# Performance work log

Hardware: AMD Instinct MI355X
Metric: run time of the kernel (lower is better)

Reference implementation:

```python
import jax, jax.numpy as jnp
import numpy as np

RADIUS = 0.5
NSAMPLE = 32
RATIO = 0.25
HEADS = 8


def _ln(x, g, b, eps=1e-5):
    m = x.mean(-1, keepdims=True)
    v = ((x - m) ** 2).mean(-1, keepdims=True)
    return (x - m) / jnp.sqrt(v + eps) * g + b


def _fps(xyz, M):
    """Farthest point sampling (start at index 0, matches pytorch3d default). Non-differentiable."""
    xyz = jax.lax.stop_gradient(xyz)  # mirrors @torch.no_grad
    B, N, _ = xyz.shape

    def step(carry, _):
        mind, last = carry  # (B,N), (B,)
        lastp = jnp.take_along_axis(xyz, last[:, None, None], axis=1)  # (B,1,3)
        d = jnp.sum((xyz - lastp) ** 2, axis=-1)  # (B,N)
        mind = jnp.minimum(mind, d)
        nxt = jnp.argmax(mind, axis=1).astype(jnp.int32)
        return (mind, nxt), last

    init = (jnp.full((B, N), jnp.inf, xyz.dtype), jnp.zeros((B,), jnp.int32))
    _, idx = jax.lax.scan(step, init, None, length=M)
    return idx.T  # (B,M)


def setup_inputs() -> dict:
    key = jax.random.key(0)
    ks = jax.random.split(key, 12)
    B, N, Cin, C = 2, 8192, 64, 128
    w = lambda i, shape: jax.random.normal(ks[i], shape, jnp.float32) * 0.02
    return {
        "xyz": jax.random.normal(ks[0], (B, N, 3), jnp.float32),
        "feats": jax.random.normal(ks[1], (B, N, Cin), jnp.float32),
        "W_in": w(2, (Cin, C)), "b_in": jnp.zeros((C,), jnp.float32),
        "ln_in_g": jnp.ones((C,), jnp.float32), "ln_in_b": jnp.zeros((C,), jnp.float32),
        "W_pos": w(3, (3, C)), "b_pos": jnp.zeros((C,), jnp.float32),
        "Wq": w(4, (C, C)), "bq": jnp.zeros((C,), jnp.float32),
        "Wk": w(5, (C, C)), "bk": jnp.zeros((C,), jnp.float32),
        "Wv": w(6, (C, C)), "bv": jnp.zeros((C,), jnp.float32),
        "Wo": w(7, (C, C)), "bo": jnp.zeros((C,), jnp.float32),
        "ln1_g": jnp.ones((C,), jnp.float32), "ln1_b": jnp.zeros((C,), jnp.float32),
        "W1": w(8, (C, 4 * C)), "b1": jnp.zeros((4 * C,), jnp.float32),
        "W2": w(9, (4 * C, C)), "b2": jnp.zeros((C,), jnp.float32),
        "ln2_g": jnp.ones((C,), jnp.float32), "ln2_b": jnp.zeros((C,), jnp.float32),
        "out_g": jnp.ones((C,), jnp.float32), "out_b": jnp.zeros((C,), jnp.float32),
    }


def reference(xyz, feats, W_in, b_in, ln_in_g, ln_in_b, W_pos, b_pos,
              Wq, bq, Wk, bk, Wv, bv, Wo, bo, ln1_g, ln1_b,
              W1, b1, W2, b2, ln2_g, ln2_b, out_g, out_b):
    B, N, _ = xyz.shape
    M = max(1, int(round(N * RATIO)))
    K = NSAMPLE

    # --- FPS centroids ---
    ctr_idx = _fps(xyz, M)  # (B,M) int32
    ctr_xyz = xyz[jnp.arange(B)[:, None], ctr_idx]  # (B,M,3)

    # --- ball query: first K points (by index) within radius; -1 where missing ---
    d2 = jnp.sum((ctr_xyz[:, :, None, :] - xyz[:, None, :, :]) ** 2, axis=-1)  # (B,M,N)
    within = d2 < RADIUS * RADIUS
    cand = jnp.where(within, jnp.arange(N, dtype=jnp.int32)[None, None, :], N)
    first_k = jnp.sort(cand, axis=-1)[..., :K]  # (B,M,K)
    raw_idx = jnp.where(first_k < N, first_k, -1)
    neigh_idx = jnp.where(raw_idx < 0, ctr_idx[:, :, None], raw_idx)  # fill pads with centroid

    b3 = jnp.arange(B)[:, None, None]
    neigh_xyz = xyz[b3, neigh_idx]     # (B,M,K,3)
    neigh_feats = feats[b3, neigh_idx]  # (B,M,K,Cin)

    # --- in_proj: Linear -> LayerNorm -> ReLU ---
    h = jax.nn.relu(_ln(neigh_feats @ W_in + b_in, ln_in_g, ln_in_b))  # (B,M,K,C)
    C = h.shape[-1]
    BM = B * M
    pad = (raw_idx < 0).reshape(BM, K)  # key padding mask

    # --- local transformer layer (coords -> positional embedding, post-norm) ---
    x = h.reshape(BM, K, C) + (neigh_xyz.reshape(BM, K, 3) @ W_pos + b_pos)
    H = HEADS
    Dh = C // H
    split = lambda t: t.reshape(BM, K, H, Dh).transpose(0, 2, 1, 3)  # (BM,H,K,Dh)
    q, k, v = split(x @ Wq + bq), split(x @ Wk + bk), split(x @ Wv + bv)
    scores = jnp.einsum('bhqd,bhkd->bhqk', q, k) / np.sqrt(Dh)
    scores = jnp.where(pad[:, None, None, :], -1e9, scores)
    attn = jax.nn.softmax(scores, axis=-1)
    o = jnp.einsum('bhqk,bhkd->bhqd', attn, v).transpose(0, 2, 1, 3).reshape(BM, K, C)
    x = _ln(x + o @ Wo + bo, ln1_g, ln1_b)
    x = _ln(x + jax.nn.relu(x @ W1 + b1) @ W2 + b2, ln2_g, ln2_b)

    # --- max-pool over neighbourhood, out LayerNorm ---
    pooled = _ln(x.max(axis=1).reshape(B, M, C), out_g, out_b)
    return ctr_xyz, pooled
```

## Files before the change

kernel.cpp:

```cpp
#include <hip/hip_runtime.h>
#include <math.h>

#define N_PTS 8192
#define BATCH 2
#define M_CTR 2048
#define KNB   32
#define CIN   64
#define CH    128
#define NHEAD 8
#define DH    16

typedef __attribute__((ext_vector_type(4))) float f32x4;
typedef __attribute__((ext_vector_type(8))) short bf16x8;

template<int CTRL>
__device__ __forceinline__ unsigned long long dpp_max_u64(unsigned long long k) {
  int lo = (int)(unsigned)k;
  int hi = (int)(k >> 32);
  int lo2 = __builtin_amdgcn_update_dpp(0, lo, CTRL, 0xF, 0xF, true);
  int hi2 = __builtin_amdgcn_update_dpp(0, hi, CTRL, 0xF, 0xF, true);
  unsigned long long o = ((unsigned long long)(unsigned)hi2 << 32) | (unsigned)lo2;
  return o > k ? o : k;
}

__device__ __forceinline__ unsigned long long swz16_max_u64(unsigned long long k) {
  int lo = (int)(unsigned)k;
  int hi = (int)(k >> 32);
  int lo2 = __builtin_amdgcn_ds_swizzle(lo, 0x401F);
  int hi2 = __builtin_amdgcn_ds_swizzle(hi, 0x401F);
  unsigned long long o = ((unsigned long long)(unsigned)hi2 << 32) | (unsigned)lo2;
  return o > k ? o : k;
}

__device__ __forceinline__ unsigned long long maxu64(unsigned long long a,
                                                     unsigned long long b) {
  return a > b ? a : b;
}

__global__ __launch_bounds__(1024, 1) void fps_kernel(const float* __restrict__ xyz,
                                                      int* __restrict__ ctrIdx,
                                                      float* __restrict__ outCtr) {
  __shared__ float4 sxyz[N_PTS];
  __shared__ unsigned long long redK[4];

  const int b = blockIdx.x;
  const int t = threadIdx.x;
  const int lane = t & 63;
  const float* xb = xyz + (size_t)b * N_PTS * 3;

  float px[8], py[8], pz[8], mind[8];
  unsigned lo8[8];
#pragma unroll
  for (int s = 0; s < 8; ++s) {
    int pt = t + s * 1024;
    float x = xb[pt * 3 + 0];
    float y = xb[pt * 3 + 1];
    float z = xb[pt * 3 + 2];
    px[s] = x; py[s] = y; pz[s] = z;
    mind[s] = INFINITY;
    lo8[s] = ~(unsigned)pt;
    sxyz[pt] = make_float4(x, y, z, 0.f);
  }
  if (t < 3) redK[t] = 0ull;
  __syncthreads();

  int last = 0;
  for (int m = 0; m < M_CTR; ++m) {
    float4 lp = sxyz[last];
    if (t == 0) {
      ctrIdx[b * M_CTR + m] = last;
      float* o = outCtr + (size_t)(b * M_CTR + m) * 3;
      o[0] = lp.x; o[1] = lp.y; o[2] = lp.z;
    }
    unsigned long long c0 = 0ull, c1 = 0ull;
#pragma unroll
    for (int s = 0; s < 8; ++s) {
      float dx = __fsub_rn(px[s], lp.x);
      float dy = __fsub_rn(py[s], lp.y);
      float dz = __fsub_rn(pz[s], lp.z);
      float d2 = __fadd_rn(__fadd_rn(__fmul_rn(dx, dx), __fmul_rn(dy, dy)),
                           __fmul_rn(dz, dz));
      float mn = fminf(mind[s], d2);
      mind[s] = mn;
      unsigned long long key =
          ((unsigned long long)__float_as_uint(mn) << 32) | lo8[s];
      if (s & 1) c1 = maxu64(c1, key); else c0 = maxu64(c0, key);
    }
    unsigned long long k0 = maxu64(c0, c1);
    k0 = dpp_max_u64<0xB1>(k0);
    k0 = dpp_max_u64<0x4E>(k0);
    k0 = dpp_max_u64<0x141>(k0);
    k0 = dpp_max_u64<0x140>(k0);
    k0 = swz16_max_u64(k0);
    const int buf = m % 3;
    if ((lane & 31) == 0)
      atomicMax((unsigned long long*)&redK[buf], k0);
    if (t == 1) redK[(m + 1) % 3] = 0ull;
    __syncthreads();
    last = (int)(~(unsigned)redK[buf]);
  }
}

__global__ __launch_bounds__(256) void ballq_kernel(const float* __restrict__ xyz,
                                                    const int* __restrict__ ctrIdx,
                                                    int* __restrict__ rawIdx) {
  const int cm   = blockIdx.x * 4 + (threadIdx.x >> 6);
  const int lane = threadIdx.x & 63;
  const int b    = cm >> 11;
  const float* xb = xyz + (size_t)b * N_PTS * 3;
  const int ci = ctrIdx[cm];
  const float cx = xb[ci * 3 + 0], cy = xb[ci * 3 + 1], cz = xb[ci * 3 + 2];
  int* out = rawIdx + (size_t)cm * KNB;
  int have = 0;
  for (int base = 0; base < N_PTS; base += 64) {
    int pt = base + lane;
    float dx = __fsub_rn(cx, xb[pt * 3 + 0]);
    float dy = __fsub_rn(cy, xb[pt * 3 + 1]);
    float dz = __fsub_rn(cz, xb[pt * 3 + 2]);
    float d2 = __fadd_rn(__fadd_rn(__fmul_rn(dx, dx), __fmul_rn(dy, dy)),
                         __fmul_rn(dz, dz));
    bool hit = d2 < 0.25f;
    unsigned long long mask = __ballot(hit);
    if (hit) {
      int rank = have + __popcll(mask & ((1ull << lane) - 1ull));
      if (rank < KNB) out[rank] = pt;
    }
    have += __popcll(mask);
    if (have >= KNB) break;
  }
  if (lane < KNB && lane >= have) out[lane] = -1;
}

__device__ __forceinline__ unsigned short f2bf(float f) {
  unsigned u = __float_as_uint(f);
  unsigned r = (u + 0x7FFFu + ((u >> 16) & 1u)) >> 16;
  return (unsigned short)r;
}
__device__ __forceinline__ float bf2f(unsigned short s) {
  return __uint_as_float(((unsigned)s) << 16);
}

__global__ __launch_bounds__(256) void prep_kernel(const float* __restrict__ W_in,
    const float* __restrict__ Wq, const float* __restrict__ Wk,
    const float* __restrict__ Wv, const float* __restrict__ Wo,
    const float* __restrict__ W1, const float* __restrict__ W2,
    short* __restrict__ wsW) {
  int i = blockIdx.x * 256 + threadIdx.x;
  if (i >= 204800) return;
  const float* src; int K, C, off;
  if (i < 8192)        { src = W_in; K = 64;  C = 128; off = i; }
  else if (i < 24576)  { src = Wq;   K = 128; C = 128; off = i - 8192; }
  else if (i < 40960)  { src = Wk;   K = 128; C = 128; off = i - 24576; }
  else if (i < 57344)  { src = Wv;   K = 128; C = 128; off = i - 40960; }
  else if (i < 73728)  { src = Wo;   K = 128; C = 128; off = i - 57344; }
  else if (i < 139264) { src = W1;   K = 128; C = 512; off = i - 73728; }
  else                 { src = W2;   K = 512; C = 128; off = i - 139264; }
  int c = off / K, k = off - c * K;
  wsW[i] = (short)f2bf(src[(size_t)k * C + c]);
}

#define XS  136
#define VTS 40
#define PS  264

struct SAParams {
  const float* xyz; const float* feats;
  const float* b_in; const float* ln_in_g; const float* ln_in_b;
  const float* W_pos; const float* b_pos;
  const float* bq; const float* bk; const float* bv; const float* bo;
  const float* ln1_g; const float* ln1_b;
  const float* b1; const float* b2;
  const float* ln2_g; const float* ln2_b; const float* out_g; const float* out_b;
  const short* wsW;
  const int* ctrIdx; const int* rawIdx;
  float* out;
};

template<int C>
__device__ __forceinline__ float dppf(float v) {
  return __int_as_float(__builtin_amdgcn_update_dpp(0, __float_as_int(v), C, 0xF, 0xF, true));
}
__device__ __forceinline__ float red16_add(float v) {
  v += dppf<0xB1>(v);  v += dppf<0x4E>(v);
  v += dppf<0x141>(v); v += dppf<0x140>(v);
  return v;
}
__device__ __forceinline__ float red16_max(float v) {
  v = fmaxf(v, dppf<0xB1>(v));  v = fmaxf(v, dppf<0x4E>(v));
  v = fmaxf(v, dppf<0x141>(v)); v = fmaxf(v, dppf<0x140>(v));
  return v;
}

template<int NCT, int NKS>
__device__ __forceinline__ void mm_mfma(const short* __restrict__ albase, int lstr,
                                        const short* __restrict__ wt, int wK,
                                        f32x4 (&acc)[NCT], int l15, int lg) {
#pragma unroll
  for (int ks = 0; ks < NKS; ++ks) {
    bf16x8 a = *(const bf16x8*)(albase + l15 * lstr + ks * 32 + lg * 8);
#pragma unroll
    for (int ct = 0; ct < NCT; ++ct) {
      bf16x8 bf = *(const bf16x8*)(wt + (size_t)(ct * 16 + l15) * wK + ks * 32 + lg * 8);
      acc[ct] = __builtin_amdgcn_mfma_f32_16x16x32_bf16(a, bf, acc[ct], 0, 0, 0);
    }
  }
}

__global__ __launch_bounds__(128, 1) void sa_kernel(SAParams p) {
  __shared__ short sm[3 * 32 * XS + 128 * VTS + 32 * PS];
  __shared__ float nxs[32], nys[32], nzs[32];
  __shared__ int   nidx[32];
  __shared__ unsigned padmaskS;
  __shared__ float psum[2][2];

  short* const xb  = sm;
  short* const qb  = sm + 32 * XS;
  short* const kb  = sm + 2 * 32 * XS;
  short* const vT  = sm + 3 * 32 * XS;
  short* const Pb  = sm + 3 * 32 * XS + 128 * VTS;
  short* const fsb = Pb;
  short* const ob  = qb;
  short* const hb  = kb;

  const int t    = threadIdx.x;
  const int lane = t & 63;
  const int rt   = t >> 6;
  const int l15  = lane & 15;
  const int lg   = lane >> 4;
  const int cm   = blockIdx.x;
  const int b    = cm >> 11;
  const short* arow = 0;

  if (t < 32) {
    int raw = p.rawIdx[(size_t)cm * KNB + t];
    int ci  = p.ctrIdx[cm];
    int ni  = (raw < 0) ? ci : raw;
    nidx[t] = ni;
    const float* q = p.xyz + ((size_t)b * N_PTS + ni) * 3;
    nxs[t] = q[0]; nys[t] = q[1]; nzs[t] = q[2];
  }
  if (t < 64) {
    bool isPad = (t < 32) ? (p.rawIdx[(size_t)cm * KNB + t] < 0) : false;
    unsigned long long m = __ballot(isPad);
    if (t == 0) padmaskS = (unsigned)m;
  }
  __syncthreads();

  {
    int row = t >> 2;
    int cs  = (t & 3) * 16;
    const float* src = p.feats + ((size_t)b * N_PTS + nidx[row]) * CIN + cs;
    float4 f0 = *(const float4*)(src + 0);
    float4 f1 = *(const float4*)(src + 4);
    float4 f2 = *(const float4*)(src + 8);
    float4 f3 = *(const float4*)(src + 12);
    unsigned short u[16];
#pragma unroll
    for (int j = 0; j < 4; ++j) {
      u[j]      = f2bf((&f0.x)[j]); u[4 + j]  = f2bf((&f1.x)[j]);
      u[8 + j]  = f2bf((&f2.x)[j]); u[12 + j] = f2bf((&f3.x)[j]);
    }
    unsigned packed[8];
#pragma unroll
    for (int j = 0; j < 8; ++j) packed[j] = (unsigned)u[2 * j] | ((unsigned)u[2 * j + 1] << 16);
    uint4 w0 = make_uint4(packed[0], packed[1], packed[2], packed[3]);
    uint4 w1 = make_uint4(packed[4], packed[5], packed[6], packed[7]);
    *(uint4*)(fsb + row * 72 + cs)     = w0;
    *(uint4*)(fsb + row * 72 + cs + 8) = w1;
  }
  __syncthreads();

  const unsigned padmask = padmaskS;
  float rowxyz[3][4];
#pragma unroll
  for (int r = 0; r < 4; ++r) {
    int row = rt * 16 + lg * 4 + r;
    rowxyz[0][r] = nxs[row]; rowxyz[1][r] = nys[row]; rowxyz[2][r] = nzs[row];
  }

  {
    f32x4 acc[8] = {};
    mm_mfma<8, 2>(fsb + rt * 16 * 72, 72, p.wsW + 0, 64, acc, l15, lg);
    float s[4] = {}, sq[4] = {};
#pragma unroll
    for (int ct = 0; ct < 8; ++ct) {
      float bia = p.b_in[ct * 16 + l15];
#pragma unroll
      for (int r = 0; r < 4; ++r) {
        acc[ct][r] += bia;
        s[r] += acc[ct][r]; sq[r] += acc[ct][r] * acc[ct][r];
      }
    }
    float mean[4], inv[4];
#pragma unroll
    for (int r = 0; r < 4; ++r) {
      float S = red16_add(s[r]), SQ = red16_add(sq[r]);
      mean[r] = S * (1.0f / CH);
      float var = fmaxf(SQ * (1.0f / CH) - mean[r] * mean[r], 0.f);
      inv[r] = rsqrtf(var + 1e-5f);
    }
#pragma unroll
    for (int ct = 0; ct < 8; ++ct) {
      int c = ct * 16 + l15;
      float g  = p.ln_in_g[c], bt = p.ln_in_b[c];
      float w0 = p.W_pos[0 * CH + c], w1 = p.W_pos[1 * CH + c];
      float w2 = p.W_pos[2 * CH + c], bp = p.b_pos[c];
#pragma unroll
      for (int r = 0; r < 4; ++r) {
        int row = rt * 16 + lg * 4 + r;
        float h = (acc[ct][r] - mean[r]) * inv[r] * g + bt;
        h = fmaxf(h, 0.f);
        float pos = fmaf(rowxyz[0][r], w0, fmaf(rowxyz[1][r], w1,
                    fmaf(rowxyz[2][r], w2, bp)));
        xb[row * XS + c] = (short)f2bf(h + pos);
      }
    }
  }
  __syncthreads();

  arow = xb + rt * 16 * XS;
  {
    f32x4 acc[8] = {};
    mm_mfma<8, 4>(arow, XS, p.wsW + 8192, 128, acc, l15, lg);
#pragma unroll
    for (int ct = 0; ct < 8; ++ct) {
      int c = ct * 16 + l15;
      float bia = p.bq[c];
#pragma unroll
      for (int r = 0; r < 4; ++r)
        qb[(rt * 16 + lg * 4 + r) * XS + c] = (short)f2bf((acc[ct][r] + bia) * 0.25f);
    }
  }
  {
    f32x4 acc[8] = {};
    mm_mfma<8, 4>(arow, XS, p.wsW + 24576, 128, acc, l15, lg);
#pragma unroll
    for (int ct = 0; ct < 8; ++ct) {
      int c = ct * 16 + l15;
      float bia = p.bk[c];
#pragma unroll
      for (int r = 0; r < 4; ++r)
        kb[(rt * 16 + lg * 4 + r) * XS + c] = (short)f2bf(acc[ct][r] + bia);
    }
  }
  {
    f32x4 acc[8] = {};
    mm_mfma<8, 4>(arow, XS, p.wsW + 40960, 128, acc, l15, lg);
#pragma unroll
    for (int ct = 0; ct < 8; ++ct) {
      int c = ct * 16 + l15;
      float bia = p.bv[c];
#pragma unroll
      for (int r = 0; r < 4; ++r)
        vT[c * VTS + rt * 16 + lg * 4 + r] = (short)f2bf(acc[ct][r] + bia);
    }
  }
  __syncthreads();

  {
    bool pad0 = (padmask >> l15) & 1u;
    bool pad1 = (padmask >> (16 + l15)) & 1u;
    const bf16x8 z = {0, 0, 0, 0, 0, 0, 0, 0};
#pragma unroll
    for (int h = 0; h < NHEAD; ++h) {
      bf16x8 a = *(const bf16x8*)(qb + (rt * 16 + l15) * XS + h * DH + (lg & 1) * 8);
      if (lg >= 2) a = z;
      bf16x8 b0 = *(const bf16x8*)(kb + (l15) * XS + h * DH + (lg & 1) * 8);
      bf16x8 b1 = *(const bf16x8*)(kb + (16 + l15) * XS + h * DH + (lg & 1) * 8);
      f32x4 s0 = {}, s1 = {};
      s0 = __builtin_amdgcn_mfma_f32_16x16x32_bf16(a, b0, s0, 0, 0, 0);
      s1 = __builtin_amdgcn_mfma_f32_16x16x32_bf16(a, b1, s1, 0, 0, 0);
#pragma unroll
      for (int r = 0; r < 4; ++r) {
        float v0 = pad0 ? -1e9f : s0[r];
        float v1 = pad1 ? -1e9f : s1[r];
        float mx = red16_max(fmaxf(v0, v1));
        float e0 = __expf(v0 - mx), e1 = __expf(v1 - mx);
        float sum = red16_add(e0 + e1);
        float isum = 1.0f / sum;
        int row = rt * 16 + lg * 4 + r;
        Pb[row * PS + h * 32 + l15]      = (short)f2bf(e0 * isum);
        Pb[row * PS + h * 32 + 16 + l15] = (short)f2bf(e1 * isum);
      }
    }
  }
  __syncthreads();

  {
#pragma unroll
    for (int h = 0; h < NHEAD; ++h) {
      bf16x8 a  = *(const bf16x8*)(Pb + (rt * 16 + l15) * PS + h * 32 + lg * 8);
      bf16x8 bf = *(const bf16x8*)(vT + (h * DH + l15) * VTS + lg * 8);
      f32x4 o = {};
      o = __builtin_amdgcn_mfma_f32_16x16x32_bf16(a, bf, o, 0, 0, 0);
#pragma unroll
      for (int r = 0; r < 4; ++r)
        ob[(rt * 16 + lg * 4 + r) * XS + h * DH + l15] = (short)f2bf(o[r]);
    }
  }

  {
    f32x4 acc[8] = {};
    mm_mfma<8, 4>(ob + rt * 16 * XS, XS, p.wsW + 57344, 128, acc, l15, lg);
    float s[4] = {}, sq[4] = {};
#pragma unroll
    for (int ct = 0; ct < 8; ++ct) {
      int c = ct * 16 + l15;
      float bia = p.bo[c];
#pragma unroll
      for (int r = 0; r < 4; ++r) {
        int row = rt * 16 + lg * 4 + r;
        acc[ct][r] += bia + bf2f((unsigned short)xb[row * XS + c]);
        s[r] += acc[ct][r]; sq[r] += acc[ct][r] * acc[ct][r];
      }
    }
    float mean[4], inv[4];
#pragma unroll
    for (int r = 0; r < 4; ++r) {
      float S = red16_add(s[r]), SQ = red16_add(sq[r]);
      mean[r] = S * (1.0f / CH);
      float var = fmaxf(SQ * (1.0f / CH) - mean[r] * mean[r], 0.f);
      inv[r] = rsqrtf(var + 1e-5f);
    }
#pragma unroll
    for (int ct = 0; ct < 8; ++ct) {
      int c = ct * 16 + l15;
      float g = p.ln1_g[c], bt = p.ln1_b[c];
#pragma unroll
      for (int r = 0; r < 4; ++r) {
        int row = rt * 16 + lg * 4 + r;
        xb[row * XS + c] = (short)f2bf((acc[ct][r] - mean[r]) * inv[r] * g + bt);
      }
    }
  }

  {
    f32x4 acc2[8] = {};
#pragma unroll
    for (int cb = 0; cb < 4; ++cb) {
      f32x4 acch[8] = {};
      mm_mfma<8, 4>(xb + rt * 16 * XS, XS, p.wsW + 73728 + cb * 128 * 128, 128,
                    acch, l15, lg);
#pragma unroll
      for (int ct = 0; ct < 8; ++ct) {
        int c = ct * 16 + l15;
        float bia = p.b1[cb * 128 + c];
#pragma unroll
        for (int r = 0; r < 4; ++r)
          hb[(rt * 16 + lg * 4 + r) * XS + c] = (short)f2bf(fmaxf(acch[ct][r] + bia, 0.f));
      }
      __syncthreads();
      mm_mfma<8, 4>(hb + rt * 16 * XS, XS, p.wsW + 139264 + cb * 128, 512,
                    acc2, l15, lg);
      __syncthreads();
    }
    float s[4] = {}, sq[4] = {};
#pragma unroll
    for (int ct = 0; ct < 8; ++ct) {
      int c = ct * 16 + l15;
      float bia = p.b2[c];
#pragma unroll
      for (int r = 0; r < 4; ++r) {
        int row = rt * 16 + lg * 4 + r;
        acc2[ct][r] += bia + bf2f((unsigned short)xb[row * XS + c]);
        s[r] += acc2[ct][r]; sq[r] += acc2[ct][r] * acc2[ct][r];
      }
    }
    float mean[4], inv[4];
#pragma unroll
    for (int r = 0; r < 4; ++r) {
      float S = red16_add(s[r]), SQ = red16_add(sq[r]);
      mean[r] = S * (1.0f / CH);
      float var = fmaxf(SQ * (1.0f / CH) - mean[r] * mean[r], 0.f);
      inv[r] = rsqrtf(var + 1e-5f);
    }
#pragma unroll
    for (int ct = 0; ct < 8; ++ct) {
      int c = ct * 16 + l15;
      float g = p.ln2_g[c], bt = p.ln2_b[c];
#pragma unroll
      for (int r = 0; r < 4; ++r) {
        int row = rt * 16 + lg * 4 + r;
        xb[row * XS + c] = (short)f2bf((acc2[ct][r] - mean[r]) * inv[r] * g + bt);
      }
    }
  }
  __syncthreads();

  {
    float mx = -INFINITY;
#pragma unroll 8
    for (int r = 0; r < KNB; ++r) mx = fmaxf(mx, bf2f((unsigned short)xb[r * XS + t]));
    float s = mx, sq = mx * mx;
#pragma unroll
    for (int off = 1; off < 64; off <<= 1) {
      s  += __shfl_xor(s,  off, 64);
      sq += __shfl_xor(sq, off, 64);
    }
    if (lane == 0) { psum[rt][0] = s; psum[rt][1] = sq; }
    __syncthreads();
    float S = psum[0][0] + psum[1][0];
    float SQ = psum[0][1] + psum[1][1];
    float mean = S * (1.0f / CH);
    float var = fmaxf(SQ * (1.0f / CH) - mean * mean, 0.f);
    float inv = rsqrtf(var + 1e-5f);
    p.out[(size_t)BATCH * M_CTR * 3 + (size_t)cm * CH + t] =
        (mx - mean) * inv * p.out_g[t] + p.out_b[t];
  }
}

extern "C" void kernel_launch(void* const* d_in, const int* in_sizes, int n_in,
                              void* d_out, int out_size, void* d_ws, size_t ws_size,
                              hipStream_t stream) {
  const float* xyz     = (const float*)d_in[0];
  const float* feats   = (const float*)d_in[1];
  const float* W_in    = (const float*)d_in[2];
  const float* b_in    = (const float*)d_in[3];
  const float* ln_in_g = (const float*)d_in[4];
  const float* ln_in_b = (const float*)d_in[5];
  const float* W_pos   = (const float*)d_in[6];
  const float* b_pos   = (const float*)d_in[7];
  const float* Wq      = (const float*)d_in[8];
  const float* bq      = (const float*)d_in[9];
  const float* Wk      = (const float*)d_in[10];
  const float* bk      = (const float*)d_in[11];
  const float* Wv      = (const float*)d_in[12];
  const float* bv      = (const float*)d_in[13];
  const float* Wo      = (const float*)d_in[14];
  const float* bo      = (const float*)d_in[15];
  const float* ln1_g   = (const float*)d_in[16];
  const float* ln1_b   = (const float*)d_in[17];
  const float* W1      = (const float*)d_in[18];
  const float* b1      = (const float*)d_in[19];
  const float* W2      = (const float*)d_in[20];
  const float* b2      = (const float*)d_in[21];
  const float* ln2_g   = (const float*)d_in[22];
  const float* ln2_b   = (const float*)d_in[23];
  const float* out_g   = (const float*)d_in[24];
  const float* out_b   = (const float*)d_in[25];
  float* out = (float*)d_out;

  int* wsCtr = (int*)d_ws;
  int* wsRaw = wsCtr + BATCH * M_CTR;
  short* wsW = (short*)(wsRaw + BATCH * M_CTR * KNB);

  prep_kernel<<<(204800 + 255) / 256, 256, 0, stream>>>(W_in, Wq, Wk, Wv, Wo,
                                                        W1, W2, wsW);
  fps_kernel<<<BATCH, 1024, 0, stream>>>(xyz, wsCtr, out);
  ballq_kernel<<<(BATCH * M_CTR) / 4, 256, 0, stream>>>(xyz, wsCtr, wsRaw);

  SAParams p{xyz, feats, b_in, ln_in_g, ln_in_b, W_pos, b_pos,
             bq, bk, bv, bo, ln1_g, ln1_b, b1, b2,
             ln2_g, ln2_b, out_g, out_b,
             wsW, wsCtr, wsRaw, out};
  sa_kernel<<<BATCH * M_CTR, 128, 0, stream>>>(p);
}
```

Measured before the change: 2.638 ms.

## Rework FPS argmax reduction with 32-bit wave reductions and per-wave LDS slots

Replaces the 64-bit packed-key DPP reduction and shared-memory atomicMax in farthest point sampling with two 32-bit wave reductions: a float max, then a min over indices among lanes holding that max. Each wave writes one packed candidate to a double-buffered LDS array, and every thread reduces the 8 candidates itself after the barrier. The block shrinks to 512 threads with 16 points per thread. The intent is to shorten the serial per-iteration critical path of the 2048 dependent FPS steps (fewer atomics, cheaper shuffles, fewer waves at the barrier), at the cost of more per-thread distance work and register use.

```diff
diff --git a/kernel.cpp b/kernel.cpp
--- a/kernel.cpp
+++ b/kernel.cpp
@@ -14,54 +14,49 @@
 typedef __attribute__((ext_vector_type(8))) short bf16x8;
 
 template<int CTRL>
-__device__ __forceinline__ unsigned long long dpp_max_u64(unsigned long long k) {
-  int lo = (int)(unsigned)k;
-  int hi = (int)(k >> 32);
-  int lo2 = __builtin_amdgcn_update_dpp(0, lo, CTRL, 0xF, 0xF, true);
-  int hi2 = __builtin_amdgcn_update_dpp(0, hi, CTRL, 0xF, 0xF, true);
-  unsigned long long o = ((unsigned long long)(unsigned)hi2 << 32) | (unsigned)lo2;
-  return o > k ? o : k;
-}
-
-__device__ __forceinline__ unsigned long long swz16_max_u64(unsigned long long k) {
-  int lo = (int)(unsigned)k;
-  int hi = (int)(k >> 32);
-  int lo2 = __builtin_amdgcn_ds_swizzle(lo, 0x401F);
-  int hi2 = __builtin_amdgcn_ds_swizzle(hi, 0x401F);
-  unsigned long long o = ((unsigned long long)(unsigned)hi2 << 32) | (unsigned)lo2;
-  return o > k ? o : k;
-}
-
+__device__ __forceinline__ float dpp_mov_f(float v) {
+  return __int_as_float(__builtin_amdgcn_update_dpp(0, __float_as_int(v), CTRL, 0xF, 0xF, true));
+}
+template<int CTRL>
+__device__ __forceinline__ unsigned dpp_mov_u(unsigned v) {
+  return (unsigned)__builtin_amdgcn_update_dpp(0, (int)v, CTRL, 0xF, 0xF, true);
+}
+__device__ __forceinline__ float swzf16(float v) {
+  return __int_as_float(__builtin_amdgcn_ds_swizzle(__float_as_int(v), 0x401F));
+}
+__device__ __forceinline__ unsigned swzu16(unsigned v) {
+  return (unsigned)__builtin_amdgcn_ds_swizzle((int)v, 0x401F);
+}
 __device__ __forceinline__ unsigned long long maxu64(unsigned long long a,
                                                      unsigned long long b) {
   return a > b ? a : b;
 }
 
-__global__ __launch_bounds__(1024, 1) void fps_kernel(const float* __restrict__ xyz,
-                                                      int* __restrict__ ctrIdx,
-                                                      float* __restrict__ outCtr) {
+__global__ __launch_bounds__(512, 1) void fps_kernel(const float* __restrict__ xyz,
+                                                     int* __restrict__ ctrIdx,
+                                                     float* __restrict__ outCtr) {
   __shared__ float4 sxyz[N_PTS];
-  __shared__ unsigned long long redK[4];
+  __shared__ __align__(16) unsigned long long candK[2][8];
 
   const int b = blockIdx.x;
   const int t = threadIdx.x;
   const int lane = t & 63;
+  const int w = t >> 6;
   const float* xb = xyz + (size_t)b * N_PTS * 3;
 
-  float px[8], py[8], pz[8], mind[8];
-  unsigned lo8[8];
-#pragma unroll
-  for (int s = 0; s < 8; ++s) {
-    int pt = t + s * 1024;
+  float px[16], py[16], pz[16], mind[16];
+  unsigned pts[16];
+#pragma unroll
+  for (int s = 0; s < 16; ++s) {
+    int pt = t + s * 512;
     float x = xb[pt * 3 + 0];
     float y = xb[pt * 3 + 1];
     float z = xb[pt * 3 + 2];
     px[s] = x; py[s] = y; pz[s] = z;
     mind[s] = INFINITY;
-    lo8[s] = ~(unsigned)pt;
+    pts[s] = (unsigned)pt;
     sxyz[pt] = make_float4(x, y, z, 0.f);
   }
-  if (t < 3) redK[t] = 0ull;
   __syncthreads();
 
   int last = 0;
@@ -72,9 +67,10 @@
       float* o = outCtr + (size_t)(b * M_CTR + m) * 3;
       o[0] = lp.x; o[1] = lp.y; o[2] = lp.z;
     }
-    unsigned long long c0 = 0ull, c1 = 0ull;
-#pragma unroll
-    for (int s = 0; s < 8; ++s) {
+    float    bv = -INFINITY;
+    unsigned bp = 0xFFFFFFFFu;
+#pragma unroll
+    for (int s = 0; s < 16; ++s) {
       float dx = __fsub_rn(px[s], lp.x);
       float dy = __fsub_rn(py[s], lp.y);
       float dz = __fsub_rn(pz[s], lp.z);
@@ -82,22 +78,34 @@
                            __fmul_rn(dz, dz));
       float mn = fminf(mind[s], d2);
       mind[s] = mn;
-      unsigned long long key =
-          ((unsigned long long)__float_as_uint(mn) << 32) | lo8[s];
-      if (s & 1) c1 = maxu64(c1, key); else c0 = maxu64(c0, key);
-    }
-    unsigned long long k0 = maxu64(c0, c1);
-    k0 = dpp_max_u64<0xB1>(k0);
-    k0 = dpp_max_u64<0x4E>(k0);
-    k0 = dpp_max_u64<0x141>(k0);
-    k0 = dpp_max_u64<0x140>(k0);
-    k0 = swz16_max_u64(k0);
-    const int buf = m % 3;
-    if ((lane & 31) == 0)
-      atomicMax((unsigned long long*)&redK[buf], k0);
-    if (t == 1) redK[(m + 1) % 3] = 0ull;
+      if (mn > bv) { bv = mn; bp = pts[s]; }
+    }
+    float gv = bv;
+    gv = fmaxf(gv, dpp_mov_f<0xB1>(gv));
+    gv = fmaxf(gv, dpp_mov_f<0x4E>(gv));
+    gv = fmaxf(gv, dpp_mov_f<0x141>(gv));
+    gv = fmaxf(gv, dpp_mov_f<0x140>(gv));
+    gv = fmaxf(gv, swzf16(gv));
+    gv = fmaxf(gv, __shfl_xor(gv, 32, 64));
+    unsigned ci = (bv == gv) ? bp : 0xFFFFFFFFu;
+    ci = min(ci, dpp_mov_u<0xB1>(ci));
+    ci = min(ci, dpp_mov_u<0x4E>(ci));
+    ci = min(ci, dpp_mov_u<0x141>(ci));
+    ci = min(ci, dpp_mov_u<0x140>(ci));
+    ci = min(ci, swzu16(ci));
+    ci = min(ci, (unsigned)__shfl_xor((int)ci, 32, 64));
+    const int buf = m & 1;
+    if (lane == 0)
+      candK[buf][w] = ((unsigned long long)__float_as_uint(gv) << 32) | ~ci;
     __syncthreads();
-    last = (int)(~(unsigned)redK[buf]);
+    const ulonglong2* ck = (const ulonglong2*)&candK[buf][0];
+    ulonglong2 c0v = ck[0], c1v = ck[1], c2v = ck[2], c3v = ck[3];
+    unsigned long long m0 = maxu64(c0v.x, c0v.y);
+    unsigned long long m1 = maxu64(c1v.x, c1v.y);
+    unsigned long long m2 = maxu64(c2v.x, c2v.y);
+    unsigned long long m3 = maxu64(c3v.x, c3v.y);
+    unsigned long long best = maxu64(maxu64(m0, m1), maxu64(m2, m3));
+    last = (int)(~(unsigned)best);
   }
 }
 
@@ -546,7 +554,7 @@
 
   prep_kernel<<<(204800 + 255) / 256, 256, 0, stream>>>(W_in, Wq, Wk, Wv, Wo,
                                                         W1, W2, wsW);
-  fps_kernel<<<BATCH, 1024, 0, stream>>>(xyz, wsCtr, out);
+  fps_kernel<<<BATCH, 512, 0, stream>>>(xyz, wsCtr, out);
   ballq_kernel<<<(BATCH * M_CTR) / 4, 256, 0, stream>>>(xyz, wsCtr, wsRaw);
 
   SAParams p{xyz, feats, b_in, ln_in_g, ln_in_b, W_pos, b_pos,
```

Measured after the change: 2.464 ms. 1.07x faster.

## Split farthest point sampling across four cooperating blocks per batch with global handshakes

Applied to the files above, without the earlier changes.

The FPS kernel now runs four 512-thread blocks per batch element instead of one 1024-thread block. Each block owns 2048 points, reduces its local argmax, publishes it to global memory with a release tag, and spin-waits for the other three blocks' candidates each iteration. The aim is to spread the serial FPS loop over more compute units and shorten the per-iteration work. The cost is a global-memory round trip and spin synchronisation on every one of 2048 iterations, and it relies on all eight blocks being co-resident.

```diff
diff --git a/kernel.cpp b/kernel.cpp
--- a/kernel.cpp
+++ b/kernel.cpp
@@ -9,6 +9,7 @@
 #define CH    128
 #define NHEAD 8
 #define DH    16
+#define FPSB  4
 
 typedef __attribute__((ext_vector_type(4))) float f32x4;
 typedef __attribute__((ext_vector_type(8))) short bf16x8;
@@ -22,7 +23,6 @@
   unsigned long long o = ((unsigned long long)(unsigned)hi2 << 32) | (unsigned)lo2;
   return o > k ? o : k;
 }
-
 __device__ __forceinline__ unsigned long long swz16_max_u64(unsigned long long k) {
   int lo = (int)(unsigned)k;
   int hi = (int)(k >> 32);
@@ -31,50 +31,63 @@
   unsigned long long o = ((unsigned long long)(unsigned)hi2 << 32) | (unsigned)lo2;
   return o > k ? o : k;
 }
-
 __device__ __forceinline__ unsigned long long maxu64(unsigned long long a,
                                                      unsigned long long b) {
   return a > b ? a : b;
 }
 
-__global__ __launch_bounds__(1024, 1) void fps_kernel(const float* __restrict__ xyz,
-                                                      int* __restrict__ ctrIdx,
-                                                      float* __restrict__ outCtr) {
+__global__ void init_sync(unsigned* __restrict__ tagG) {
+  if (threadIdx.x < BATCH * FPSB) tagG[threadIdx.x] = 0u;
+}
+
+__global__ __launch_bounds__(512, 1) void fps_kernel(const float* __restrict__ xyz,
+                                                     int* __restrict__ ctrIdx,
+                                                     float* __restrict__ outCtr,
+                                                     unsigned long long* __restrict__ candG,
+                                                     unsigned* __restrict__ tagG) {
   __shared__ float4 sxyz[N_PTS];
-  __shared__ unsigned long long redK[4];
-
-  const int b = blockIdx.x;
+  __shared__ __align__(16) unsigned long long candK[8];
+  __shared__ unsigned long long remC[3];
+
+  const int gb  = blockIdx.x;
+  const int b   = gb >> 2;
+  const int blk = gb & 3;
   const int t = threadIdx.x;
   const int lane = t & 63;
+  const int w = t >> 6;
   const float* xb = xyz + (size_t)b * N_PTS * 3;
 
-  float px[8], py[8], pz[8], mind[8];
-  unsigned lo8[8];
-#pragma unroll
-  for (int s = 0; s < 8; ++s) {
-    int pt = t + s * 1024;
-    float x = xb[pt * 3 + 0];
-    float y = xb[pt * 3 + 1];
-    float z = xb[pt * 3 + 2];
-    px[s] = x; py[s] = y; pz[s] = z;
+  for (int i = t; i < N_PTS; i += 512)
+    sxyz[i] = make_float4(xb[i * 3 + 0], xb[i * 3 + 1], xb[i * 3 + 2], 0.f);
+
+  float px[4], py[4], pz[4], mind[4];
+  unsigned lo4[4];
+#pragma unroll
+  for (int s = 0; s < 4; ++s) {
+    int pt = blk * 2048 + s * 512 + t;
+    px[s] = xb[pt * 3 + 0];
+    py[s] = xb[pt * 3 + 1];
+    pz[s] = xb[pt * 3 + 2];
     mind[s] = INFINITY;
-    lo8[s] = ~(unsigned)pt;
-    sxyz[pt] = make_float4(x, y, z, 0.f);
-  }
-  if (t < 3) redK[t] = 0ull;
-  __syncthreads();
+    lo4[s] = ~(unsigned)pt;
+  }
+  __syncthreads();
+
+  unsigned long long* myCand0 = candG + (size_t)(b * 2 + 0) * FPSB;
+  unsigned long long* myCand1 = candG + (size_t)(b * 2 + 1) * FPSB;
+  unsigned* myTag = tagG + b * FPSB;
 
   int last = 0;
   for (int m = 0; m < M_CTR; ++m) {
     float4 lp = sxyz[last];
-    if (t == 0) {
+    if (blk == 0 && t == 0) {
       ctrIdx[b * M_CTR + m] = last;
       float* o = outCtr + (size_t)(b * M_CTR + m) * 3;
       o[0] = lp.x; o[1] = lp.y; o[2] = lp.z;
     }
-    unsigned long long c0 = 0ull, c1 = 0ull;
-#pragma unroll
-    for (int s = 0; s < 8; ++s) {
+    unsigned long long key[4];
+#pragma unroll
+    for (int s = 0; s < 4; ++s) {
       float dx = __fsub_rn(px[s], lp.x);
       float dy = __fsub_rn(py[s], lp.y);
       float dz = __fsub_rn(pz[s], lp.z);
@@ -82,22 +95,44 @@
                            __fmul_rn(dz, dz));
       float mn = fminf(mind[s], d2);
       mind[s] = mn;
-      unsigned long long key =
-          ((unsigned long long)__float_as_uint(mn) << 32) | lo8[s];
-      if (s & 1) c1 = maxu64(c1, key); else c0 = maxu64(c0, key);
-    }
-    unsigned long long k0 = maxu64(c0, c1);
+      key[s] = ((unsigned long long)__float_as_uint(mn) << 32) | lo4[s];
+    }
+    key[0] = maxu64(key[0], key[2]);
+    key[1] = maxu64(key[1], key[3]);
+    unsigned long long k0 = maxu64(key[0], key[1]);
     k0 = dpp_max_u64<0xB1>(k0);
     k0 = dpp_max_u64<0x4E>(k0);
     k0 = dpp_max_u64<0x141>(k0);
     k0 = dpp_max_u64<0x140>(k0);
     k0 = swz16_max_u64(k0);
-    const int buf = m % 3;
-    if ((lane & 31) == 0)
-      atomicMax((unsigned long long*)&redK[buf], k0);
-    if (t == 1) redK[(m + 1) % 3] = 0ull;
+    k0 = maxu64(k0, (unsigned long long)__shfl_xor((unsigned long long)k0, 32, 64));
+    if (lane == 0) candK[w] = k0;
     __syncthreads();
-    last = (int)(~(unsigned)redK[buf]);
+    const ulonglong2* ck = (const ulonglong2*)&candK[0];
+    ulonglong2 c0v = ck[0], c1v = ck[1], c2v = ck[2], c3v = ck[3];
+    unsigned long long m0 = maxu64(c0v.x, c0v.y);
+    unsigned long long m1 = maxu64(c1v.x, c1v.y);
+    unsigned long long m2 = maxu64(c2v.x, c2v.y);
+    unsigned long long m3 = maxu64(c3v.x, c3v.y);
+    unsigned long long blockBest = maxu64(maxu64(m0, m1), maxu64(m2, m3));
+    unsigned long long* candPar = (m & 1) ? myCand1 : myCand0;
+    if (t == 0) {
+      __hip_atomic_store(&candPar[blk], blockBest, __ATOMIC_RELAXED,
+                         __HIP_MEMORY_SCOPE_AGENT);
+      __hip_atomic_store(&myTag[blk], (unsigned)(m + 1), __ATOMIC_RELEASE,
+                         __HIP_MEMORY_SCOPE_AGENT);
+    }
+    if (t < 3) {
+      int j = (blk + 1 + t) & 3;
+      while (__hip_atomic_load(&myTag[j], __ATOMIC_ACQUIRE,
+                               __HIP_MEMORY_SCOPE_AGENT) < (unsigned)(m + 1)) {}
+      remC[t] = __hip_atomic_load(&candPar[j], __ATOMIC_RELAXED,
+                                  __HIP_MEMORY_SCOPE_AGENT);
+    }
+    __syncthreads();
+    unsigned long long best = maxu64(maxu64(blockBest, remC[0]),
+                                     maxu64(remC[1], remC[2]));
+    last = (int)(~(unsigned)best);
   }
 }
 
@@ -542,11 +577,15 @@
 
   int* wsCtr = (int*)d_ws;
   int* wsRaw = wsCtr + BATCH * M_CTR;
-  short* wsW = (short*)(wsRaw + BATCH * M_CTR * KNB);
-
+  unsigned long long* candG =
+      (unsigned long long*)(wsRaw + BATCH * M_CTR * KNB);
+  unsigned* tagG = (unsigned*)(candG + 2 * BATCH * FPSB);
+  short* wsW = (short*)(tagG + BATCH * FPSB);
+
+  init_sync<<<1, 64, 0, stream>>>(tagG);
   prep_kernel<<<(204800 + 255) / 256, 256, 0, stream>>>(W_in, Wq, Wk, Wv, Wo,
                                                         W1, W2, wsW);
-  fps_kernel<<<BATCH, 1024, 0, stream>>>(xyz, wsCtr, out);
+  fps_kernel<<<BATCH * FPSB, 512, 0, stream>>>(xyz, wsCtr, out, candG, tagG);
   ballq_kernel<<<(BATCH * M_CTR) / 4, 256, 0, stream>>>(xyz, wsCtr, wsRaw);
 
   SAParams p{xyz, feats, b_in, ln_in_g, ln_in_b, W_pos, b_pos,
```

Result: slower. 4.776 ms (+81.1%).
